# Kernel tuning notes

Hardware: AMD Instinct MI355X
Metric: run time of the kernel (lower is better)

## Reference

```python
import jax, jax.numpy as jnp
import numpy as np

WSZ = 8
HEADS = 8
FILTER_RATE = 0.3
EPS = 1e-5


def layer_norm(x, w, b):
    mu = x.mean(-1, keepdims=True)
    var = ((x - mu) ** 2).mean(-1, keepdims=True)
    return (x - mu) * jax.lax.rsqrt(var + EPS) * w + b


def setup_inputs() -> dict:
    key = jax.random.key(0)
    ks = jax.random.split(key, 8)
    B, C, H, W = 2, 256, 512, 512
    C2 = 2 * C
    s = 0.02
    return {
        "feature_map": jax.random.normal(ks[0], (B, C, H, W), jnp.float32),
        "uncertain_map": jax.random.uniform(ks[1], (B, H, W), jnp.float32),
        "norm_w": jnp.ones((C,), jnp.float32),
        "norm_b": jnp.zeros((C,), jnp.float32),
        "lin0_w": jax.random.normal(ks[2], (C, C2), jnp.float32) * s,
        "lin0_b": jnp.zeros((C2,), jnp.float32),
        "qkv0_w": jax.random.normal(ks[3], (C2, 3 * C2), jnp.float32) * s,
        "lin1_w": jax.random.normal(ks[4], (C2, C2), jnp.float32) * s,
        "lin1_b": jnp.zeros((C2,), jnp.float32),
        "qkv1_w": jax.random.normal(ks[5], (C2, 3 * C2), jnp.float32) * s,
        "proj_w": jax.random.normal(ks[6], (C2, C), jnp.float32) * s,
        "proj_b": jnp.zeros((C,), jnp.float32),
    }


def _window_attn(xf, qkv_w, scale, winsz, C2):
    # xf: (N, winsz, C2)
    qkv = (xf @ qkv_w).reshape(-1, winsz, 3, HEADS, C2 // HEADS)
    q, k, v = qkv[:, :, 0], qkv[:, :, 1], qkv[:, :, 2]  # (N, winsz, H, dh)
    a = jnp.einsum("nqhd,nkhd->nhqk", q, k) * scale
    a = jax.nn.softmax(a, axis=-1)
    o = jnp.einsum("nhqk,nkhd->nqhd", a, v).reshape(-1, winsz, C2)
    return xf + o


def reference(feature_map, uncertain_map, norm_w, norm_b, lin0_w, lin0_b,
              qkv0_w, lin1_w, lin1_b, qkv1_w, proj_w, proj_b):
    B, C, H, W = feature_map.shape
    wsz = WSZ
    nH, nW = H // wsz, W // wsz
    nWin, winsz = nH * nW, wsz * wsz
    nWF = int(nWin * FILTER_RATE)
    C2 = 2 * C
    scale = (C // HEADS) ** -0.5  # module uses C//num_heads, not C2//num_heads

    # window partition
    x = jnp.transpose(feature_map, (0, 2, 3, 1))  # B H W C
    win_x = x.reshape(B, nH, wsz, nW, wsz, C).transpose(0, 1, 3, 2, 4, 5)
    win_x = win_x.reshape(B * nWin, winsz, C)
    win_unc = uncertain_map.reshape(B, nH, wsz, nW, wsz).transpose(0, 1, 3, 2, 4)
    win_unc = win_unc.reshape(B, nWin, winsz)

    # topk window selection by mean uncertainty
    score = win_unc.mean(-1)  # (B, nWin)
    _, idx = jax.lax.top_k(score, nWF)  # (B, nWF)
    flat_idx = (idx + jnp.arange(B)[:, None] * nWin).reshape(-1)  # (B*nWF,)

    xw = win_x[flat_idx]  # gather: (B*nWF, winsz, C)
    xn = layer_norm(xw, norm_w, norm_b)

    # local branch: repeat 0
    xf = jax.nn.gelu(xn @ lin0_w + lin0_b, approximate=False)
    xf = _window_attn(xf, qkv0_w, scale, winsz, C2)
    # repeat 1
    xf = xf + jax.nn.gelu(xf @ lin1_w + lin1_b, approximate=False)
    xf = _window_attn(xf, qkv1_w, scale, winsz, C2)

    out_f = xn + jax.nn.gelu(xf @ proj_w + proj_b, approximate=False)

    # scatter-add back into unnormalized windows
    win_x = win_x.at[flat_idx].add(out_f)

    x = win_x.reshape(B, nH, nW, wsz, wsz, C).transpose(0, 1, 3, 2, 4, 5)
    x = x.reshape(B, H, W, C)
    return jnp.transpose(x, (0, 3, 1, 2))
```

## Files before the change

kernel.cpp:

```cpp
#include <hip/hip_runtime.h>
#include <math.h>

typedef unsigned short u16;
typedef unsigned int   u32;
typedef __attribute__((ext_vector_type(8))) short bf16x8;
typedef __attribute__((ext_vector_type(4))) float f32x4;

#define DEV static __device__ __forceinline__

DEV u16 f2b(float f) {
  union { float f; u32 u; } v; v.f = f;
  u32 r = v.u + 0x7FFFu + ((v.u >> 16) & 1u);
  return (u16)(r >> 16);
}
DEV float b2f(u16 h) {
  union { u32 u; float f; } v; v.u = ((u32)h) << 16;
  return v.f;
}
DEV float gelu_f(float x) { return 0.5f * x * (1.0f + erff(x * 0.70710678118654752f)); }

DEV void gload16(const u16* g, u16* l) {
  __builtin_amdgcn_global_load_lds(
      (const __attribute__((address_space(1))) void*)g,
      (__attribute__((address_space(3))) void*)l, 16, 0, 0);
}

__global__ void k_transpose_w(const float* __restrict__ src, u16* __restrict__ dst,
                              int K, int N) {
  long t = (long)blockIdx.x * 256 + threadIdx.x;
  if (t >= (long)K * N) return;
  int n = (int)(t / K), k = (int)(t % K);
  dst[t] = f2b(src[(long)k * N + n]);
}

__global__ void k_scores(const float* __restrict__ unc, float* __restrict__ scores) {
  int id = blockIdx.x * 256 + threadIdx.x;
  if (id >= 8192) return;
  int b = id >> 12, win = id & 4095;
  int h0 = (win >> 6) << 3, w0 = (win & 63) << 3;
  float r[8] = {0.f,0.f,0.f,0.f,0.f,0.f,0.f,0.f};
  for (int i = 0; i < 8; ++i) {
    long base = ((long)(b * 512 + h0 + i)) * 512 + w0;
    #pragma unroll
    for (int j = 0; j < 8; ++j) r[j] += unc[base + j];
  }
  float s = ((r[0] + r[1]) + (r[2] + r[3])) + ((r[4] + r[5]) + (r[6] + r[7]));
  scores[id] = s * (1.0f / 64.0f);
}

__global__ __launch_bounds__(1024) void k_topk(
    const float* __restrict__ scores, int* __restrict__ row2win,
    int* __restrict__ win2row, int nWF) {
  __shared__ float ls[4096];
  __shared__ int   li[4096];
  const int b = blockIdx.x;
  const int tid = threadIdx.x;
  for (int i = tid; i < 4096; i += 1024) {
    ls[i] = scores[b * 4096 + i];
    li[i] = i;
    win2row[b * 4096 + i] = -1;
  }
  __syncthreads();
  for (int k = 2; k <= 4096; k <<= 1) {
    for (int j = k >> 1; j > 0; j >>= 1) {
      for (int t = tid; t < 2048; t += 1024) {
        int i = ((t / j) * (j << 1)) + (t % j);
        int ixj = i + j;
        bool up = ((i & k) == 0);
        float sa = ls[i], sb = ls[ixj];
        int ia = li[i], ib = li[ixj];
        bool g = (sa > sb) || (sa == sb && ia < ib);
        if (g != up) { ls[i] = sb; ls[ixj] = sa; li[i] = ib; li[ixj] = ia; }
      }
      __syncthreads();
    }
  }
  for (int r = tid; r < nWF; r += 1024) {
    int win = li[r];
    row2win[b * nWF + r] = (b << 12) | win;
    win2row[b * 4096 + win] = b * nWF + r;
  }
}

__global__ __launch_bounds__(256) void k_gather_ln(
    const float* __restrict__ fm, const float* __restrict__ nw,
    const float* __restrict__ nb, const int* __restrict__ row2win,
    u16* __restrict__ xn, int winStart) {
  __shared__ float sx[64 * 256];
  const int tid = threadIdx.x;
  const int rw = row2win[winStart + blockIdx.x];
  const int b = rw >> 12, win = rw & 4095;
  const int h0 = (win >> 6) << 3, w0 = (win & 63) << 3;
  {
    const int c8 = tid >> 3, h = tid & 7;
    #pragma unroll
    for (int cc = 0; cc < 8; ++cc) {
      const int c = cc * 32 + c8;
      long base = ((long)(b * 256 + c) * 512 + h0 + h) * 512 + w0;
      float4 v0 = *(const float4*)(fm + base);
      float4 v1 = *(const float4*)(fm + base + 4);
      float vv[8] = {v0.x, v0.y, v0.z, v0.w, v1.x, v1.y, v1.z, v1.w};
      #pragma unroll
      for (int j = 0; j < 8; ++j) {
        int tok = h * 8 + j;
        sx[tok * 256 + (c ^ ((tok & 15) << 1))] = vv[j];
      }
    }
  }
  __syncthreads();
  const int tok = tid >> 2, g = tid & 3;
  const int swz = (tok & 15) << 1;
  float sum = 0.f;
  for (int q = 0; q < 64; ++q) sum += sx[tok * 256 + ((g * 64 + q) ^ swz)];
  sum += __shfl_xor(sum, 1);
  sum += __shfl_xor(sum, 2);
  const float mu = sum * (1.0f / 256.0f);
  float s2 = 0.f;
  for (int q = 0; q < 64; ++q) {
    float d = sx[tok * 256 + ((g * 64 + q) ^ swz)] - mu;
    s2 += d * d;
  }
  s2 += __shfl_xor(s2, 1);
  s2 += __shfl_xor(s2, 2);
  const float rs = rsqrtf(s2 * (1.0f / 256.0f) + 1e-5f);
  long obase = ((long)blockIdx.x * 64 + tok) * 256 + g * 64;
  for (int q8 = 0; q8 < 8; ++q8) {
    u16 tmp[8];
    #pragma unroll
    for (int e = 0; e < 8; ++e) {
      int c = g * 64 + q8 * 8 + e;
      float v = (sx[tok * 256 + (c ^ swz)] - mu) * rs * nw[c] + nb[c];
      tmp[e] = f2b(v);
    }
    *(ulonglong2*)(xn + obase + q8 * 8) = *(const ulonglong2*)tmp;
  }
}

template <int EPI, int NT, int KD>
__global__ __launch_bounds__(512, 2) void k_gemm256(
    const u16* __restrict__ A, const u16* __restrict__ Bt,
    const float* __restrict__ bias, const u16* __restrict__ Res,
    u16* __restrict__ Y, int N, int nWork) {
  constexpr int NKT = KD / 64;
  constexpr int LG_NKT = (KD == 512) ? 3 : 2;
  constexpr int NIP = KD / 128;
  constexpr int LG_NIP = (KD == 512) ? 2 : 1;
  __shared__ __attribute__((aligned(16))) u16 S[65536];
  __shared__ __attribute__((aligned(16))) u16 E[16384];
  const int tid = threadIdx.x;
  const int l = tid & 63, wid = tid >> 6;
  const int wm = wid >> 2, wn = wid & 3;

  const int slot = ((blockIdx.x & 7) << 5) | (blockIdx.x >> 3);
  const int q = nWork >> 8, rr = nWork & 255;
  const int wrkBase = slot * q + (slot < rr ? slot : rr);
  const int myN = q + (slot < rr ? 1 : 0);
  if (myN == 0) return;

  const int srow = wid * 8 + (l >> 3);
  const int k0b = ((l & 7) << 4) ^ ((l >> 3) << 4);
  const int vko = k0b >> 1;
  char* ldsS = (char*)S + wid * 1024 + l * 16;
  const char* Sb = (const char*)S;

  f32x4 acc[8][4] = {};
  bf16x8 bfrag[4][2];
  bf16x8 af[2][2];

#define STG(G, ISB, H) do { \
    const int wig_ = (G) >> LG_NKT; \
    const int ktg_ = (G) & (NKT - 1); \
    const int wrkg_ = wrkBase + wig_; \
    const int tmg_ = wrkg_ / NT, tng_ = wrkg_ % NT; \
    const u16* g_ = (ISB) ? Bt + (long)(tng_ * 256 + srow) * KD + vko \
                          : A + (long)(tmg_ * 256 + srow) * KD + vko; \
    char* lp_ = ldsS + ((G) & 1) * 65536 + (ISB) * 32768 + (H) * 16384; \
    gload16(g_ + (long)((H) * 128) * KD + ktg_ * 64, (u16*)lp_); \
    gload16(g_ + (long)((H) * 128 + 64) * KD + ktg_ * 64, (u16*)(lp_ + 8192)); \
  } while (0)

#define DS_B(T) do { \
    _Pragma("unroll") for (int ni_ = 0; ni_ < 4; ++ni_) { \
      const int r_ = wn * 64 + ni_ * 16 + (l & 15); \
      _Pragma("unroll") for (int kk_ = 0; kk_ < 2; ++kk_) { \
        const int kb_ = kk_ * 64 + ((l >> 4) << 4); \
        bfrag[ni_][kk_] = *(const bf16x8*)(Sb + ((T) & 1) * 65536 + 32768 + r_ * 128 + (kb_ ^ ((r_ & 7) << 4))); \
      } } \
  } while (0)

#define DS_A(T, Q) do { \
    _Pragma("unroll") for (int m2_ = 0; m2_ < 2; ++m2_) { \
      const int r_ = wm * 128 + (2 * (Q) + m2_) * 16 + (l & 15); \
      _Pragma("unroll") for (int kk_ = 0; kk_ < 2; ++kk_) { \
        const int kb_ = kk_ * 64 + ((l >> 4) << 4); \
        af[m2_][kk_] = *(const bf16x8*)(Sb + ((T) & 1) * 65536 + r_ * 128 + (kb_ ^ ((r_ & 7) << 4))); \
      } } \
  } while (0)

#define MFMA16(Q) do { \
    _Pragma("unroll") for (int m2_ = 0; m2_ < 2; ++m2_) \
      _Pragma("unroll") for (int ni_ = 0; ni_ < 4; ++ni_) \
        _Pragma("unroll") for (int kk_ = 0; kk_ < 2; ++kk_) \
          acc[2 * (Q) + m2_][ni_] = __builtin_amdgcn_mfma_f32_16x16x32_bf16( \
              af[m2_][kk_], bfrag[ni_][kk_], acc[2 * (Q) + m2_][ni_], 0, 0, 0); \
  } while (0)

#define BAR_MFMA(Q) do { \
    __builtin_amdgcn_s_barrier(); \
    asm volatile("s_waitcnt lgkmcnt(0)" ::: "memory"); \
    __builtin_amdgcn_sched_barrier(0); \
    __builtin_amdgcn_s_setprio(1); \
    MFMA16(Q); \
    __builtin_amdgcn_s_setprio(0); \
  } while (0)

#define PH_END() do { \
    __builtin_amdgcn_s_barrier(); \
    __builtin_amdgcn_sched_barrier(0); \
  } while (0)

  STG(0, 0, 0); STG(0, 0, 1); STG(0, 1, 0); STG(0, 1, 1);
  STG(1, 0, 0); STG(1, 0, 1); STG(1, 1, 0); STG(1, 1, 1);
  asm volatile("s_waitcnt vmcnt(8)" ::: "memory");
  __builtin_amdgcn_s_barrier();
  __builtin_amdgcn_sched_barrier(0);

  const int giEnd = myN * NIP;
  for (int gi = 0; gi < giEnd; ++gi) {
    const int t0 = 2 * gi, t1 = t0 + 1;
    const bool more = (gi + 1 < giEnd);
    DS_B(t0); DS_A(t0, 0);
    if (gi > 0) STG(t1, 0, 0);
    BAR_MFMA(0); PH_END();
    DS_A(t0, 1);
    if (gi > 0) STG(t1, 0, 1);
    if (more) STG(t0 + 2, 1, 0);
    BAR_MFMA(1); PH_END();
    DS_A(t0, 2);
    if (more) STG(t0 + 2, 1, 1);
    BAR_MFMA(2); PH_END();
    DS_A(t0, 3);
    BAR_MFMA(3);
    if (more) { asm volatile("s_waitcnt vmcnt(4)" ::: "memory"); }
    else      { asm volatile("s_waitcnt vmcnt(0)" ::: "memory"); }
    PH_END();
    DS_B(t1); DS_A(t1, 0);
    if (more) STG(t0 + 2, 0, 0);
    BAR_MFMA(0); PH_END();
    DS_A(t1, 1);
    if (more) STG(t0 + 2, 0, 1);
    BAR_MFMA(1); PH_END();
    DS_A(t1, 2);
    if (more) STG(t1 + 2, 1, 0);
    BAR_MFMA(2); PH_END();
    DS_A(t1, 3);
    if (more) STG(t1 + 2, 1, 1);
    BAR_MFMA(3);
    if (more) { asm volatile("s_waitcnt vmcnt(4)" ::: "memory"); }
    PH_END();

    if (((gi + 1) & (NIP - 1)) == 0) {
      const int wrk = wrkBase + (gi >> LG_NIP);
      const int tm = wrk / NT, tn = wrk % NT;
      if (EPI == 3) {
        float bv[4];
        #pragma unroll
        for (int ni = 0; ni < 4; ++ni)
          bv[ni] = bias[tn * 256 + wn * 64 + ni * 16 + (l & 15)];
        const long rbase = (long)tm * 256 + wm * 128 + ((l >> 4) << 2);
        const int cbase = tn * 256 + wn * 64 + (l & 15);
        #pragma unroll
        for (int mi = 0; mi < 8; ++mi) {
          #pragma unroll
          for (int r = 0; r < 4; ++r) {
            long m = rbase + mi * 16 + r;
            #pragma unroll
            for (int ni = 0; ni < 4; ++ni) {
              int n = cbase + ni * 16;
              float v = gelu_f(acc[mi][ni][r] + bv[ni]);
              v += b2f(Res[m * N + n]);
              Y[((m >> 6) * 256 + n) * 64 + (m & 63)] = f2b(v);
            }
          }
        }
      } else {
        float bv[4];
        if (EPI == 1 || EPI == 2) {
          #pragma unroll
          for (int ni = 0; ni < 4; ++ni)
            bv[ni] = bias[tn * 256 + wn * 64 + ni * 16 + (l & 15)];
        }
        #pragma unroll
        for (int sw = 0; sw < 4; ++sw) {
          #pragma unroll
          for (int mi2 = 0; mi2 < 2; ++mi2) {
            const int mi = 2 * sw + mi2;
            const int lr0 = wm * 32 + mi2 * 16 + ((l >> 4) << 2);
            #pragma unroll
            for (int r = 0; r < 4; ++r) {
              const int lrr = lr0 + r;
              #pragma unroll
              for (int ni = 0; ni < 4; ++ni) {
                float v = acc[mi][ni][r];
                if (EPI == 1 || EPI == 2) v = gelu_f(v + bv[ni]);
                const int col = wn * 64 + ni * 16 + (l & 15);
                E[lrr * 256 + ((((col >> 3) ^ (lrr & 7)) << 3) | (col & 7))] = f2b(v);
              }
            }
          }
          asm volatile("s_waitcnt lgkmcnt(0)" ::: "memory");
          __builtin_amdgcn_s_barrier();
          const int lr2 = tid >> 3;
          const long m = (long)tm * 256 + (lr2 >> 5) * 128 + sw * 32 + (lr2 & 31);
          #pragma unroll
          for (int rd = 0; rd < 4; ++rd) {
            const int chunk = rd * 8 + (tid & 7);
            ulonglong2 val = *(const ulonglong2*)(E + lr2 * 256 + ((chunk ^ (lr2 & 7)) << 3));
            const int n = tn * 256 + chunk * 8;
            if (EPI == 2) {
              u16 tv[8], rv[8];
              *(ulonglong2*)tv = val;
              *(ulonglong2*)rv = *(const ulonglong2*)(Res + m * N + n);
              #pragma unroll
              for (int e = 0; e < 8; ++e) tv[e] = f2b(b2f(tv[e]) + b2f(rv[e]));
              val = *(const ulonglong2*)tv;
            }
            if (EPI == 4) {
              const long win = m >> 6;
              const int t_ = n >> 9, h_ = (n >> 6) & 7, d0 = n & 63;
              *(ulonglong2*)(Y + ((((win * 8 + h_) * 3 + t_) * 64 + (m & 63)) * 64 + d0)) = val;
            } else {
              *(ulonglong2*)(Y + m * N + n) = val;
            }
          }
          if (sw < 3) {
            __builtin_amdgcn_s_barrier();
          }
        }
      }
      #pragma unroll
      for (int mi = 0; mi < 8; ++mi)
        #pragma unroll
        for (int ni = 0; ni < 4; ++ni)
          acc[mi][ni] = (f32x4){0.f, 0.f, 0.f, 0.f};
    }
  }
#undef STG
#undef DS_B
#undef DS_A
#undef MFMA16
#undef BAR_MFMA
#undef PH_END
}

__global__ __launch_bounds__(256) void k_attn(
    const u16* __restrict__ qkv, u16* __restrict__ xf) {
  __shared__ __attribute__((aligned(16))) u16 sq[64 * 64];
  __shared__ __attribute__((aligned(16))) u16 sk[64 * 64];
  __shared__ __attribute__((aligned(16))) u16 sv[64 * 64];
  __shared__ __attribute__((aligned(16))) u16 sp[64 * 64];
  const int tid = threadIdx.x;
  const int l = tid & 63, w = tid >> 6;
  const int wloc = blockIdx.x >> 3, h = blockIdx.x & 7;
  const long tokbase = (long)wloc * 64;
  const u16* base = qkv + (long)blockIdx.x * 12288;

  #pragma unroll
  for (int rd = 0; rd < 6; ++rd) {
    const int cid = rd * 256 + tid;
    ulonglong2 v16 = *(const ulonglong2*)(base + (long)cid * 8);
    const int t = (cid >> 3) & 63, d0 = (cid & 7) << 3;
    if (rd < 2) {
      *(ulonglong2*)((char*)sq + t * 128 + ((d0 * 2) ^ ((t & 7) << 4))) = v16;
    } else if (rd < 4) {
      *(ulonglong2*)((char*)sk + t * 128 + ((d0 * 2) ^ ((t & 7) << 4))) = v16;
    } else {
      u16 vv[8];
      *(ulonglong2*)vv = v16;
      #pragma unroll
      for (int e = 0; e < 8; ++e) {
        int r = d0 + e;
        *(u16*)((char*)sv + r * 128 + ((t * 2) ^ ((r & 7) << 4))) = vv[e];
      }
    }
  }
  __syncthreads();

  f32x4 accs[4] = {};
  #pragma unroll
  for (int ks = 0; ks < 2; ++ks) {
    int kb = ks * 64 + ((l >> 4) << 4);
    int ra = w * 16 + (l & 15);
    bf16x8 aq = *(const bf16x8*)((char*)sq + ra * 128 + (kb ^ ((ra & 7) << 4)));
    #pragma unroll
    for (int cf = 0; cf < 4; ++cf) {
      int rb = cf * 16 + (l & 15);
      bf16x8 bk = *(const bf16x8*)((char*)sk + rb * 128 + (kb ^ ((rb & 7) << 4)));
      accs[cf] = __builtin_amdgcn_mfma_f32_16x16x32_bf16(aq, bk, accs[cf], 0, 0, 0);
    }
  }
  const float scale = 0.17677669529663687f;
  float pv[4][4];
  #pragma unroll
  for (int r = 0; r < 4; ++r) {
    float m = -1e30f;
    #pragma unroll
    for (int cf = 0; cf < 4; ++cf) {
      pv[cf][r] = accs[cf][r] * scale;
      m = fmaxf(m, pv[cf][r]);
    }
    for (int off = 1; off < 16; off <<= 1) m = fmaxf(m, __shfl_xor(m, off));
    float s = 0.f;
    #pragma unroll
    for (int cf = 0; cf < 4; ++cf) { pv[cf][r] = __expf(pv[cf][r] - m); s += pv[cf][r]; }
    for (int off = 1; off < 16; off <<= 1) s += __shfl_xor(s, off);
    float inv = 1.0f / s;
    #pragma unroll
    for (int cf = 0; cf < 4; ++cf) pv[cf][r] *= inv;
  }
  #pragma unroll
  for (int cf = 0; cf < 4; ++cf)
    #pragma unroll
    for (int r = 0; r < 4; ++r) {
      int pr = w * 16 + ((l >> 4) << 2) + r, pc = cf * 16 + (l & 15);
      *(u16*)((char*)sp + pr * 128 + ((pc * 2) ^ ((pr & 7) << 4))) = f2b(pv[cf][r]);
    }
  __syncthreads();

  f32x4 acco[4] = {};
  #pragma unroll
  for (int ks = 0; ks < 2; ++ks) {
    int kb = ks * 64 + ((l >> 4) << 4);
    int ra = w * 16 + (l & 15);
    bf16x8 ap = *(const bf16x8*)((char*)sp + ra * 128 + (kb ^ ((ra & 7) << 4)));
    #pragma unroll
    for (int cf = 0; cf < 4; ++cf) {
      int rb = cf * 16 + (l & 15);
      bf16x8 bvv = *(const bf16x8*)((char*)sv + rb * 128 + (kb ^ ((rb & 7) << 4)));
      acco[cf] = __builtin_amdgcn_mfma_f32_16x16x32_bf16(ap, bvv, acco[cf], 0, 0, 0);
    }
  }
  #pragma unroll
  for (int cf = 0; cf < 4; ++cf)
    #pragma unroll
    for (int r = 0; r < 4; ++r) {
      long m = tokbase + w * 16 + ((l >> 4) << 2) + r;
      int n = h * 64 + cf * 16 + (l & 15);
      long idx = m * 512 + n;
      xf[idx] = f2b(acco[cf][r] + b2f(xf[idx]));
    }
}

__global__ __launch_bounds__(256) void k_assemble(
    const float* __restrict__ fm, const u16* __restrict__ out_f,
    const int* __restrict__ win2row, float* __restrict__ out) {
  const int tid = threadIdx.x;
  const int bq = blockIdx.x;
  const int hw = bq & 63, c = (bq >> 6) & 255, b = bq >> 14;
  const int w0 = (tid & 127) << 2;
  const int hlo = tid >> 7;
  const int win = hw * 64 + (w0 >> 3);
  const int r = win2row[b * 4096 + win];
  const u16* ofb = out_f + ((long)(r < 0 ? 0 : r) * 256 + c) * 64 + (w0 & 7);
  const long base = ((long)(b * 256 + c) * 512 + hw * 8) * 512 + w0;
  #pragma unroll
  for (int jj = 0; jj < 4; ++jj) {
    const int h = jj * 2 + hlo;
    float4 v = *(const float4*)(fm + base + (long)h * 512);
    if (r >= 0) {
      ushort4 ov = *(const ushort4*)(ofb + h * 8);
      v.x += b2f(ov.x);
      v.y += b2f(ov.y);
      v.z += b2f(ov.z);
      v.w += b2f(ov.w);
    }
    *(float4*)(out + base + (long)h * 512) = v;
  }
}

extern "C" void kernel_launch(void* const* d_in, const int* in_sizes, int n_in,
                              void* d_out, int out_size, void* d_ws, size_t ws_size,
                              hipStream_t stream) {
  const float* fm     = (const float*)d_in[0];
  const float* unc    = (const float*)d_in[1];
  const float* nw     = (const float*)d_in[2];
  const float* nb     = (const float*)d_in[3];
  const float* w_lin0 = (const float*)d_in[4];
  const float* b_lin0 = (const float*)d_in[5];
  const float* w_qkv0 = (const float*)d_in[6];
  const float* w_lin1 = (const float*)d_in[7];
  const float* b_lin1 = (const float*)d_in[8];
  const float* w_qkv1 = (const float*)d_in[9];
  const float* w_proj = (const float*)d_in[10];
  const float* b_proj = (const float*)d_in[11];
  float* out = (float*)d_out;

  const int nWF = 1228, totWin = 2456;
  const long totTok = (long)totWin * 64;

  char* p = (char*)d_ws;
  auto alloc = [&](size_t bytes) {
    char* r = p;
    p += (bytes + 255) & ~(size_t)255;
    return r;
  };
  float* scores = (float*)alloc(8192 * 4);
  int* win2row  = (int*)alloc(8192 * 4);
  int* row2win  = (int*)alloc(totWin * 4);
  u16* wT       = (u16*)alloc((size_t)2097152 * 2);
  u16* out_f    = (u16*)alloc((size_t)(totTok + 256) * 256 * 2);
  size_t persist = (size_t)(p - (char*)d_ws);

  int wpc = totWin;
  {
    const int cands[6] = {1, 2, 4, 8, 16, 32};
    for (int ci = 0; ci < 6; ++ci) {
      int n = cands[ci];
      int wp = ((totWin + n - 1) / n + 3) & ~3;
      size_t mc = (size_t)wp * 64;
      size_t need = persist + 4096 +
                    ((mc * 256 * 2 + 255) & ~(size_t)255) +
                    2 * ((mc * 512 * 2 + 255) & ~(size_t)255) +
                    ((mc * 1536 * 2 + 255) & ~(size_t)255);
      if (need <= ws_size) { wpc = wp; break; }
    }
  }
  long mcap = (long)wpc * 64;
  u16* xn   = (u16*)alloc((size_t)mcap * 256 * 2);
  u16* xfa  = (u16*)alloc((size_t)mcap * 512 * 2);
  u16* xfb  = (u16*)alloc((size_t)mcap * 512 * 2);
  u16* qkvb = (u16*)alloc((size_t)mcap * 1536 * 2);

  u16* wT_lin0 = wT;
  u16* wT_qkv0 = wT + 131072;
  u16* wT_lin1 = wT + 917504;
  u16* wT_qkv1 = wT + 1179648;
  u16* wT_proj = wT + 1966080;
  k_transpose_w<<<(131072 + 255) / 256, 256, 0, stream>>>(w_lin0, wT_lin0, 256, 512);
  k_transpose_w<<<(786432 + 255) / 256, 256, 0, stream>>>(w_qkv0, wT_qkv0, 512, 1536);
  k_transpose_w<<<(262144 + 255) / 256, 256, 0, stream>>>(w_lin1, wT_lin1, 512, 512);
  k_transpose_w<<<(786432 + 255) / 256, 256, 0, stream>>>(w_qkv1, wT_qkv1, 512, 1536);
  k_transpose_w<<<(131072 + 255) / 256, 256, 0, stream>>>(w_proj, wT_proj, 512, 256);

  k_scores<<<32, 256, 0, stream>>>(unc, scores);
  k_topk<<<2, 1024, 0, stream>>>(scores, row2win, win2row, nWF);

  for (int w0 = 0; w0 < totWin; w0 += wpc) {
    int rem = totWin - w0;
    int wn = (wpc < rem) ? wpc : rem;
    int mT = wn / 4;
    k_gather_ln<<<wn, 256, 0, stream>>>(fm, nw, nb, row2win, xn, w0);
    k_gemm256<1, 2, 256><<<256, 512, 0, stream>>>(xn, wT_lin0, b_lin0, nullptr, xfa, 512, mT * 2);
    k_gemm256<4, 6, 512><<<256, 512, 0, stream>>>(xfa, wT_qkv0, nullptr, nullptr, qkvb, 1536, mT * 6);
    k_attn<<<wn * 8, 256, 0, stream>>>(qkvb, xfa);
    k_gemm256<2, 2, 512><<<256, 512, 0, stream>>>(xfa, wT_lin1, b_lin1, xfa, xfb, 512, mT * 2);
    k_gemm256<4, 6, 512><<<256, 512, 0, stream>>>(xfb, wT_qkv1, nullptr, nullptr, qkvb, 1536, mT * 6);
    k_attn<<<wn * 8, 256, 0, stream>>>(qkvb, xfb);
    k_gemm256<3, 1, 512><<<256, 512, 0, stream>>>(xfb, wT_proj, b_proj, xn,
                                                  out_f + (long)w0 * 16384, 256, mT * 1);
  }
  k_assemble<<<32768, 256, 0, stream>>>(fm, out_f, win2row, out);
}
```

Before: 1.983 ms.

## Replace persistent 256x256 pipelined GEMM with simple 128x128 one-tile-per-block GEMM

Replaces the persistent 512-thread GEMM, which used 256x256 tiles, a double-buffered LDS pipeline and multi-phase barriers, with a 256-thread kernel. The new kernel computes one 128x128 tile per block over a single-buffered K loop, and the grid is sized to the number of tiles with an XCD-aware block remap. The aim is more parallelism and occupancy from smaller tiles and lower LDS use. The cost is less operand reuse per tile and no overlap of global loads with MFMA, since each K step waits for its loads to finish before the barrier.

```diff
diff --git a/kernel.cpp b/kernel.cpp
--- a/kernel.cpp
+++ b/kernel.cpp
@@ -137,220 +137,151 @@
 }
 
 template <int EPI, int NT, int KD>
-__global__ __launch_bounds__(512, 2) void k_gemm256(
+__global__ __launch_bounds__(256, 3) void k_gemm128(
     const u16* __restrict__ A, const u16* __restrict__ Bt,
     const float* __restrict__ bias, const u16* __restrict__ Res,
-    u16* __restrict__ Y, int N, int nWork) {
+    u16* __restrict__ Y, int N) {
+  __shared__ __attribute__((aligned(16))) u16 S[16384];
+  const int tid = threadIdx.x;
+  const int l = tid & 63, w = tid >> 6;
+  const int wm = w >> 1, wn = w & 1;
+
+  const int nwg = gridDim.x;
+  const int dd = blockIdx.x;
+  const int xcd = dd & 7, jb = dd >> 3;
+  const int q = nwg >> 3, r8 = nwg & 7;
+  const int wrk = (xcd < r8 ? xcd * (q + 1) : r8 * (q + 1) + (xcd - r8) * q) + jb;
+  const int tm = wrk / NT, tn = wrk % NT;
+
+  const int k0b = ((l & 7) << 4) ^ ((l >> 3) << 4);
+  const u16* gA = A + (long)(tm * 128 + w * 8 + (l >> 3)) * KD + (k0b >> 1);
+  const u16* gB = Bt + (long)(tn * 128 + w * 8 + (l >> 3)) * KD + (k0b >> 1);
+  u16* lA = S + w * 512 + l * 8;
+  u16* lB = lA + 8192;
+  const char* Sb = (const char*)S;
+
+  f32x4 acc[4][4] = {};
   constexpr int NKT = KD / 64;
-  constexpr int LG_NKT = (KD == 512) ? 3 : 2;
-  constexpr int NIP = KD / 128;
-  constexpr int LG_NIP = (KD == 512) ? 2 : 1;
-  __shared__ __attribute__((aligned(16))) u16 S[65536];
-  __shared__ __attribute__((aligned(16))) u16 E[16384];
-  const int tid = threadIdx.x;
-  const int l = tid & 63, wid = tid >> 6;
-  const int wm = wid >> 2, wn = wid & 3;
-
-  const int slot = ((blockIdx.x & 7) << 5) | (blockIdx.x >> 3);
-  const int q = nWork >> 8, rr = nWork & 255;
-  const int wrkBase = slot * q + (slot < rr ? slot : rr);
-  const int myN = q + (slot < rr ? 1 : 0);
-  if (myN == 0) return;
-
-  const int srow = wid * 8 + (l >> 3);
-  const int k0b = ((l & 7) << 4) ^ ((l >> 3) << 4);
-  const int vko = k0b >> 1;
-  char* ldsS = (char*)S + wid * 1024 + l * 16;
-  const char* Sb = (const char*)S;
-
-  f32x4 acc[8][4] = {};
-  bf16x8 bfrag[4][2];
-  bf16x8 af[2][2];
-
-#define STG(G, ISB, H) do { \
-    const int wig_ = (G) >> LG_NKT; \
-    const int ktg_ = (G) & (NKT - 1); \
-    const int wrkg_ = wrkBase + wig_; \
-    const int tmg_ = wrkg_ / NT, tng_ = wrkg_ % NT; \
-    const u16* g_ = (ISB) ? Bt + (long)(tng_ * 256 + srow) * KD + vko \
-                          : A + (long)(tmg_ * 256 + srow) * KD + vko; \
-    char* lp_ = ldsS + ((G) & 1) * 65536 + (ISB) * 32768 + (H) * 16384; \
-    gload16(g_ + (long)((H) * 128) * KD + ktg_ * 64, (u16*)lp_); \
-    gload16(g_ + (long)((H) * 128 + 64) * KD + ktg_ * 64, (u16*)(lp_ + 8192)); \
+
+#define STAGE128(KT) do { \
+    _Pragma("unroll") for (int jr_ = 0; jr_ < 4; ++jr_) { \
+      gload16(gA + (long)jr_ * 32 * KD + (KT) * 64, lA + jr_ * 2048); \
+      gload16(gB + (long)jr_ * 32 * KD + (KT) * 64, lB + jr_ * 2048); \
+    } \
   } while (0)
 
-#define DS_B(T) do { \
-    _Pragma("unroll") for (int ni_ = 0; ni_ < 4; ++ni_) { \
-      const int r_ = wn * 64 + ni_ * 16 + (l & 15); \
-      _Pragma("unroll") for (int kk_ = 0; kk_ < 2; ++kk_) { \
-        const int kb_ = kk_ * 64 + ((l >> 4) << 4); \
-        bfrag[ni_][kk_] = *(const bf16x8*)(Sb + ((T) & 1) * 65536 + 32768 + r_ * 128 + (kb_ ^ ((r_ & 7) << 4))); \
-      } } \
-  } while (0)
-
-#define DS_A(T, Q) do { \
-    _Pragma("unroll") for (int m2_ = 0; m2_ < 2; ++m2_) { \
-      const int r_ = wm * 128 + (2 * (Q) + m2_) * 16 + (l & 15); \
-      _Pragma("unroll") for (int kk_ = 0; kk_ < 2; ++kk_) { \
-        const int kb_ = kk_ * 64 + ((l >> 4) << 4); \
-        af[m2_][kk_] = *(const bf16x8*)(Sb + ((T) & 1) * 65536 + r_ * 128 + (kb_ ^ ((r_ & 7) << 4))); \
-      } } \
-  } while (0)
-
-#define MFMA16(Q) do { \
-    _Pragma("unroll") for (int m2_ = 0; m2_ < 2; ++m2_) \
-      _Pragma("unroll") for (int ni_ = 0; ni_ < 4; ++ni_) \
-        _Pragma("unroll") for (int kk_ = 0; kk_ < 2; ++kk_) \
-          acc[2 * (Q) + m2_][ni_] = __builtin_amdgcn_mfma_f32_16x16x32_bf16( \
-              af[m2_][kk_], bfrag[ni_][kk_], acc[2 * (Q) + m2_][ni_], 0, 0, 0); \
-  } while (0)
-
-#define BAR_MFMA(Q) do { \
-    __builtin_amdgcn_s_barrier(); \
-    asm volatile("s_waitcnt lgkmcnt(0)" ::: "memory"); \
-    __builtin_amdgcn_sched_barrier(0); \
-    __builtin_amdgcn_s_setprio(1); \
-    MFMA16(Q); \
-    __builtin_amdgcn_s_setprio(0); \
-  } while (0)
-
-#define PH_END() do { \
-    __builtin_amdgcn_s_barrier(); \
-    __builtin_amdgcn_sched_barrier(0); \
-  } while (0)
-
-  STG(0, 0, 0); STG(0, 0, 1); STG(0, 1, 0); STG(0, 1, 1);
-  STG(1, 0, 0); STG(1, 0, 1); STG(1, 1, 0); STG(1, 1, 1);
-  asm volatile("s_waitcnt vmcnt(8)" ::: "memory");
+  STAGE128(0);
+  asm volatile("s_waitcnt vmcnt(0)" ::: "memory");
   __builtin_amdgcn_s_barrier();
   __builtin_amdgcn_sched_barrier(0);
 
-  const int giEnd = myN * NIP;
-  for (int gi = 0; gi < giEnd; ++gi) {
-    const int t0 = 2 * gi, t1 = t0 + 1;
-    const bool more = (gi + 1 < giEnd);
-    DS_B(t0); DS_A(t0, 0);
-    if (gi > 0) STG(t1, 0, 0);
-    BAR_MFMA(0); PH_END();
-    DS_A(t0, 1);
-    if (gi > 0) STG(t1, 0, 1);
-    if (more) STG(t0 + 2, 1, 0);
-    BAR_MFMA(1); PH_END();
-    DS_A(t0, 2);
-    if (more) STG(t0 + 2, 1, 1);
-    BAR_MFMA(2); PH_END();
-    DS_A(t0, 3);
-    BAR_MFMA(3);
-    if (more) { asm volatile("s_waitcnt vmcnt(4)" ::: "memory"); }
-    else      { asm volatile("s_waitcnt vmcnt(0)" ::: "memory"); }
-    PH_END();
-    DS_B(t1); DS_A(t1, 0);
-    if (more) STG(t0 + 2, 0, 0);
-    BAR_MFMA(0); PH_END();
-    DS_A(t1, 1);
-    if (more) STG(t0 + 2, 0, 1);
-    BAR_MFMA(1); PH_END();
-    DS_A(t1, 2);
-    if (more) STG(t1 + 2, 1, 0);
-    BAR_MFMA(2); PH_END();
-    DS_A(t1, 3);
-    if (more) STG(t1 + 2, 1, 1);
-    BAR_MFMA(3);
-    if (more) { asm volatile("s_waitcnt vmcnt(4)" ::: "memory"); }
-    PH_END();
-
-    if (((gi + 1) & (NIP - 1)) == 0) {
-      const int wrk = wrkBase + (gi >> LG_NIP);
-      const int tm = wrk / NT, tn = wrk % NT;
-      if (EPI == 3) {
-        float bv[4];
+  for (int kt = 0; kt < NKT; ++kt) {
+    bf16x8 af[4][2], bf[4][2];
+    #pragma unroll
+    for (int mi = 0; mi < 4; ++mi) {
+      const int r_ = wm * 64 + mi * 16 + (l & 15);
+      #pragma unroll
+      for (int kk = 0; kk < 2; ++kk) {
+        const int kb = kk * 64 + ((l >> 4) << 4);
+        af[mi][kk] = *(const bf16x8*)(Sb + r_ * 128 + (kb ^ ((r_ & 7) << 4)));
+      }
+    }
+    #pragma unroll
+    for (int ni = 0; ni < 4; ++ni) {
+      const int r_ = wn * 64 + ni * 16 + (l & 15);
+      #pragma unroll
+      for (int kk = 0; kk < 2; ++kk) {
+        const int kb = kk * 64 + ((l >> 4) << 4);
+        bf[ni][kk] = *(const bf16x8*)(Sb + 16384 + r_ * 128 + (kb ^ ((r_ & 7) << 4)));
+      }
+    }
+    asm volatile("s_waitcnt lgkmcnt(0)" ::: "memory");
+    __builtin_amdgcn_sched_barrier(0);
+    __builtin_amdgcn_s_barrier();
+    __builtin_amdgcn_sched_barrier(0);
+    if (kt + 1 < NKT) STAGE128(kt + 1);
+    #pragma unroll
+    for (int mi = 0; mi < 4; ++mi)
+      #pragma unroll
+      for (int ni = 0; ni < 4; ++ni)
         #pragma unroll
-        for (int ni = 0; ni < 4; ++ni)
-          bv[ni] = bias[tn * 256 + wn * 64 + ni * 16 + (l & 15)];
-        const long rbase = (long)tm * 256 + wm * 128 + ((l >> 4) << 2);
-        const int cbase = tn * 256 + wn * 64 + (l & 15);
+        for (int kk = 0; kk < 2; ++kk)
+          acc[mi][ni] = __builtin_amdgcn_mfma_f32_16x16x32_bf16(
+              af[mi][kk], bf[ni][kk], acc[mi][ni], 0, 0, 0);
+    if (kt + 1 < NKT) {
+      asm volatile("s_waitcnt vmcnt(0)" ::: "memory");
+      __builtin_amdgcn_s_barrier();
+      __builtin_amdgcn_sched_barrier(0);
+    }
+  }
+
+  if (EPI == 3) {
+    float bv[4];
+    #pragma unroll
+    for (int ni = 0; ni < 4; ++ni)
+      bv[ni] = bias[tn * 128 + wn * 64 + ni * 16 + (l & 15)];
+    #pragma unroll
+    for (int mi = 0; mi < 4; ++mi) {
+      #pragma unroll
+      for (int r = 0; r < 4; ++r) {
+        long m = (long)tm * 128 + wm * 64 + mi * 16 + ((l >> 4) << 2) + r;
         #pragma unroll
-        for (int mi = 0; mi < 8; ++mi) {
-          #pragma unroll
-          for (int r = 0; r < 4; ++r) {
-            long m = rbase + mi * 16 + r;
-            #pragma unroll
-            for (int ni = 0; ni < 4; ++ni) {
-              int n = cbase + ni * 16;
-              float v = gelu_f(acc[mi][ni][r] + bv[ni]);
-              v += b2f(Res[m * N + n]);
-              Y[((m >> 6) * 256 + n) * 64 + (m & 63)] = f2b(v);
-            }
-          }
+        for (int ni = 0; ni < 4; ++ni) {
+          int n = tn * 128 + wn * 64 + ni * 16 + (l & 15);
+          float v = gelu_f(acc[mi][ni][r] + bv[ni]);
+          v += b2f(Res[m * N + n]);
+          Y[((m >> 6) * 256 + n) * 64 + (m & 63)] = f2b(v);
         }
+      }
+    }
+  } else {
+    float bv[4];
+    if (EPI == 1 || EPI == 2) {
+      #pragma unroll
+      for (int ni = 0; ni < 4; ++ni)
+        bv[ni] = bias[tn * 128 + wn * 64 + ni * 16 + (l & 15)];
+    }
+    #pragma unroll
+    for (int mi = 0; mi < 4; ++mi) {
+      #pragma unroll
+      for (int r = 0; r < 4; ++r) {
+        const int row = wm * 64 + mi * 16 + ((l >> 4) << 2) + r;
+        #pragma unroll
+        for (int ni = 0; ni < 4; ++ni) {
+          float v = acc[mi][ni][r];
+          if (EPI == 1 || EPI == 2) v = gelu_f(v + bv[ni]);
+          const int col = wn * 64 + ni * 16 + (l & 15);
+          *(u16*)((char*)S + row * 256 + ((col * 2) ^ ((row & 7) << 4))) = f2b(v);
+        }
+      }
+    }
+    asm volatile("s_waitcnt lgkmcnt(0)" ::: "memory");
+    __builtin_amdgcn_s_barrier();
+    const int row = tid >> 1, half = tid & 1;
+    const long m = (long)tm * 128 + row;
+    #pragma unroll
+    for (int jr = 0; jr < 8; ++jr) {
+      ulonglong2 val = *(const ulonglong2*)(
+          Sb + row * 256 + ((half * 128 + jr * 16) ^ ((row & 7) << 4)));
+      const int n = tn * 128 + half * 64 + jr * 8;
+      if (EPI == 2) {
+        u16 tv[8], rv[8];
+        *(ulonglong2*)tv = val;
+        *(ulonglong2*)rv = *(const ulonglong2*)(Res + m * N + n);
+        #pragma unroll
+        for (int e = 0; e < 8; ++e) tv[e] = f2b(b2f(tv[e]) + b2f(rv[e]));
+        val = *(const ulonglong2*)tv;
+      }
+      if (EPI == 4) {
+        const long win = m >> 6;
+        const int t_ = n >> 9, h_ = (n >> 6) & 7, d0 = n & 63;
+        *(ulonglong2*)(Y + ((((win * 8 + h_) * 3 + t_) * 64 + (m & 63)) * 64 + d0)) = val;
       } else {
-        float bv[4];
-        if (EPI == 1 || EPI == 2) {
-          #pragma unroll
-          for (int ni = 0; ni < 4; ++ni)
-            bv[ni] = bias[tn * 256 + wn * 64 + ni * 16 + (l & 15)];
-        }
-        #pragma unroll
-        for (int sw = 0; sw < 4; ++sw) {
-          #pragma unroll
-          for (int mi2 = 0; mi2 < 2; ++mi2) {
-            const int mi = 2 * sw + mi2;
-            const int lr0 = wm * 32 + mi2 * 16 + ((l >> 4) << 2);
-            #pragma unroll
-            for (int r = 0; r < 4; ++r) {
-              const int lrr = lr0 + r;
-              #pragma unroll
-              for (int ni = 0; ni < 4; ++ni) {
-                float v = acc[mi][ni][r];
-                if (EPI == 1 || EPI == 2) v = gelu_f(v + bv[ni]);
-                const int col = wn * 64 + ni * 16 + (l & 15);
-                E[lrr * 256 + ((((col >> 3) ^ (lrr & 7)) << 3) | (col & 7))] = f2b(v);
-              }
-            }
-          }
-          asm volatile("s_waitcnt lgkmcnt(0)" ::: "memory");
-          __builtin_amdgcn_s_barrier();
-          const int lr2 = tid >> 3;
-          const long m = (long)tm * 256 + (lr2 >> 5) * 128 + sw * 32 + (lr2 & 31);
-          #pragma unroll
-          for (int rd = 0; rd < 4; ++rd) {
-            const int chunk = rd * 8 + (tid & 7);
-            ulonglong2 val = *(const ulonglong2*)(E + lr2 * 256 + ((chunk ^ (lr2 & 7)) << 3));
-            const int n = tn * 256 + chunk * 8;
-            if (EPI == 2) {
-              u16 tv[8], rv[8];
-              *(ulonglong2*)tv = val;
-              *(ulonglong2*)rv = *(const ulonglong2*)(Res + m * N + n);
-              #pragma unroll
-              for (int e = 0; e < 8; ++e) tv[e] = f2b(b2f(tv[e]) + b2f(rv[e]));
-              val = *(const ulonglong2*)tv;
-            }
-            if (EPI == 4) {
-              const long win = m >> 6;
-              const int t_ = n >> 9, h_ = (n >> 6) & 7, d0 = n & 63;
-              *(ulonglong2*)(Y + ((((win * 8 + h_) * 3 + t_) * 64 + (m & 63)) * 64 + d0)) = val;
-            } else {
-              *(ulonglong2*)(Y + m * N + n) = val;
-            }
-          }
-          if (sw < 3) {
-            __builtin_amdgcn_s_barrier();
-          }
-        }
-      }
-      #pragma unroll
-      for (int mi = 0; mi < 8; ++mi)
-        #pragma unroll
-        for (int ni = 0; ni < 4; ++ni)
-          acc[mi][ni] = (f32x4){0.f, 0.f, 0.f, 0.f};
-    }
-  }
-#undef STG
-#undef DS_B
-#undef DS_A
-#undef MFMA16
-#undef BAR_MFMA
-#undef PH_END
+        *(ulonglong2*)(Y + m * N + n) = val;
+      }
+    }
+  }
+#undef STAGE128
 }
 
 __global__ __launch_bounds__(256) void k_attn(
@@ -548,16 +479,16 @@
   for (int w0 = 0; w0 < totWin; w0 += wpc) {
     int rem = totWin - w0;
     int wn = (wpc < rem) ? wpc : rem;
-    int mT = wn / 4;
+    int mT = wn / 2;
     k_gather_ln<<<wn, 256, 0, stream>>>(fm, nw, nb, row2win, xn, w0);
-    k_gemm256<1, 2, 256><<<256, 512, 0, stream>>>(xn, wT_lin0, b_lin0, nullptr, xfa, 512, mT * 2);
-    k_gemm256<4, 6, 512><<<256, 512, 0, stream>>>(xfa, wT_qkv0, nullptr, nullptr, qkvb, 1536, mT * 6);
+    k_gemm128<1, 4, 256><<<mT * 4, 256, 0, stream>>>(xn, wT_lin0, b_lin0, nullptr, xfa, 512);
+    k_gemm128<4, 12, 512><<<mT * 12, 256, 0, stream>>>(xfa, wT_qkv0, nullptr, nullptr, qkvb, 1536);
     k_attn<<<wn * 8, 256, 0, stream>>>(qkvb, xfa);
-    k_gemm256<2, 2, 512><<<256, 512, 0, stream>>>(xfa, wT_lin1, b_lin1, xfa, xfb, 512, mT * 2);
-    k_gemm256<4, 6, 512><<<256, 512, 0, stream>>>(xfb, wT_qkv1, nullptr, nullptr, qkvb, 1536, mT * 6);
+    k_gemm128<2, 4, 512><<<mT * 4, 256, 0, stream>>>(xfa, wT_lin1, b_lin1, xfa, xfb, 512);
+    k_gemm128<4, 12, 512><<<mT * 12, 256, 0, stream>>>(xfb, wT_qkv1, nullptr, nullptr, qkvb, 1536);
     k_attn<<<wn * 8, 256, 0, stream>>>(qkvb, xfb);
-    k_gemm256<3, 1, 512><<<256, 512, 0, stream>>>(xfb, wT_proj, b_proj, xn,
-                                                  out_f + (long)w0 * 16384, 256, mT * 1);
+    k_gemm128<3, 2, 512><<<mT * 2, 256, 0, stream>>>(xfb, wT_proj, b_proj, xn,
+                                                     out_f + (long)w0 * 16384, 256);
   }
   k_assemble<<<32768, 256, 0, stream>>>(fm, out_f, win2row, out);
 }
```

New measurement: 2.130 ms. +7.4%, slower.

## Replace persistent GEMM scheduling with one tile per workgroup grid

Applied to the files above, without the earlier changes.

The GEMM kernel no longer runs as a persistent 256-block grid that loops over several output tiles with a cross-tile prefetch pipeline. It now launches one workgroup per 256x256 tile, mapped so that consecutive tiles land on the same XCD. The separate epilogue LDS buffer E is dropped and the staging buffer S is reused, which cuts LDS per block and may allow more blocks resident. In exchange, the kernel loses the prefetch of the next tile's operands across tile boundaries and adds launch and tail costs when the tile count is not a multiple of the CU count.

```diff
diff --git a/kernel.cpp b/kernel.cpp
--- a/kernel.cpp
+++ b/kernel.cpp
@@ -140,26 +140,23 @@
 __global__ __launch_bounds__(512, 2) void k_gemm256(
     const u16* __restrict__ A, const u16* __restrict__ Bt,
     const float* __restrict__ bias, const u16* __restrict__ Res,
-    u16* __restrict__ Y, int N, int nWork) {
-  constexpr int NKT = KD / 64;
-  constexpr int LG_NKT = (KD == 512) ? 3 : 2;
-  constexpr int NIP = KD / 128;
-  constexpr int LG_NIP = (KD == 512) ? 2 : 1;
+    u16* __restrict__ Y, int N) {
   __shared__ __attribute__((aligned(16))) u16 S[65536];
-  __shared__ __attribute__((aligned(16))) u16 E[16384];
   const int tid = threadIdx.x;
   const int l = tid & 63, wid = tid >> 6;
   const int wm = wid >> 2, wn = wid & 3;
 
-  const int slot = ((blockIdx.x & 7) << 5) | (blockIdx.x >> 3);
-  const int q = nWork >> 8, rr = nWork & 255;
-  const int wrkBase = slot * q + (slot < rr ? slot : rr);
-  const int myN = q + (slot < rr ? 1 : 0);
-  if (myN == 0) return;
+  const int nwg = gridDim.x;
+  const int d = blockIdx.x;
+  const int xcd = d & 7, j = d >> 3;
+  const int q = nwg >> 3, r8 = nwg & 7;
+  const int wrk = (xcd < r8 ? xcd * (q + 1) : r8 * (q + 1) + (xcd - r8) * q) + j;
+  const int tm = wrk / NT, tn = wrk % NT;
 
   const int srow = wid * 8 + (l >> 3);
   const int k0b = ((l & 7) << 4) ^ ((l >> 3) << 4);
-  const int vko = k0b >> 1;
+  const u16* gA = A + (long)(tm * 256 + srow) * KD + (k0b >> 1);
+  const u16* gB = Bt + (long)(tn * 256 + srow) * KD + (k0b >> 1);
   char* ldsS = (char*)S + wid * 1024 + l * 16;
   const char* Sb = (const char*)S;
 
@@ -167,16 +164,11 @@
   bf16x8 bfrag[4][2];
   bf16x8 af[2][2];
 
-#define STG(G, ISB, H) do { \
-    const int wig_ = (G) >> LG_NKT; \
-    const int ktg_ = (G) & (NKT - 1); \
-    const int wrkg_ = wrkBase + wig_; \
-    const int tmg_ = wrkg_ / NT, tng_ = wrkg_ % NT; \
-    const u16* g_ = (ISB) ? Bt + (long)(tng_ * 256 + srow) * KD + vko \
-                          : A + (long)(tmg_ * 256 + srow) * KD + vko; \
-    char* lp_ = ldsS + ((G) & 1) * 65536 + (ISB) * 32768 + (H) * 16384; \
-    gload16(g_ + (long)((H) * 128) * KD + ktg_ * 64, (u16*)lp_); \
-    gload16(g_ + (long)((H) * 128 + 64) * KD + ktg_ * 64, (u16*)(lp_ + 8192)); \
+#define STG(T, ISB, H) do { \
+    const u16* g_ = (ISB) ? gB : gA; \
+    char* lp_ = ldsS + ((T) & 1) * 65536 + (ISB) * 32768 + (H) * 16384; \
+    gload16(g_ + (long)((H) * 128) * KD + (long)(T) * 64, (u16*)lp_); \
+    gload16(g_ + (long)((H) * 128 + 64) * KD + (long)(T) * 64, (u16*)(lp_ + 8192)); \
   } while (0)
 
 #define DS_B(T) do { \
@@ -225,15 +217,15 @@
   __builtin_amdgcn_s_barrier();
   __builtin_amdgcn_sched_barrier(0);
 
-  const int giEnd = myN * NIP;
-  for (int gi = 0; gi < giEnd; ++gi) {
-    const int t0 = 2 * gi, t1 = t0 + 1;
-    const bool more = (gi + 1 < giEnd);
+  constexpr int nIter = KD >> 7;
+  for (int i = 0; i < nIter; ++i) {
+    const int t0 = 2 * i, t1 = 2 * i + 1;
+    const bool more = (i + 1 < nIter);
     DS_B(t0); DS_A(t0, 0);
-    if (gi > 0) STG(t1, 0, 0);
+    if (i > 0) STG(t1, 0, 0);
     BAR_MFMA(0); PH_END();
     DS_A(t0, 1);
-    if (gi > 0) STG(t1, 0, 1);
+    if (i > 0) STG(t1, 0, 1);
     if (more) STG(t0 + 2, 1, 0);
     BAR_MFMA(1); PH_END();
     DS_A(t0, 2);
@@ -258,91 +250,82 @@
     BAR_MFMA(3);
     if (more) { asm volatile("s_waitcnt vmcnt(4)" ::: "memory"); }
     PH_END();
-
-    if (((gi + 1) & (NIP - 1)) == 0) {
-      const int wrk = wrkBase + (gi >> LG_NIP);
-      const int tm = wrk / NT, tn = wrk % NT;
-      if (EPI == 3) {
-        float bv[4];
+  }
+
+  if (EPI == 3) {
+    float bv[4];
+    #pragma unroll
+    for (int ni = 0; ni < 4; ++ni)
+      bv[ni] = bias[tn * 256 + wn * 64 + ni * 16 + (l & 15)];
+    const long rbase = (long)tm * 256 + wm * 128 + ((l >> 4) << 2);
+    const int cbase = tn * 256 + wn * 64 + (l & 15);
+    #pragma unroll
+    for (int mi = 0; mi < 8; ++mi) {
+      #pragma unroll
+      for (int r = 0; r < 4; ++r) {
+        long m = rbase + mi * 16 + r;
         #pragma unroll
-        for (int ni = 0; ni < 4; ++ni)
-          bv[ni] = bias[tn * 256 + wn * 64 + ni * 16 + (l & 15)];
-        const long rbase = (long)tm * 256 + wm * 128 + ((l >> 4) << 2);
-        const int cbase = tn * 256 + wn * 64 + (l & 15);
+        for (int ni = 0; ni < 4; ++ni) {
+          int n = cbase + ni * 16;
+          float v = gelu_f(acc[mi][ni][r] + bv[ni]);
+          v += b2f(Res[m * N + n]);
+          Y[((m >> 6) * 256 + n) * 64 + (m & 63)] = f2b(v);
+        }
+      }
+    }
+  } else {
+    float bv[4];
+    if (EPI == 1 || EPI == 2) {
+      #pragma unroll
+      for (int ni = 0; ni < 4; ++ni)
+        bv[ni] = bias[tn * 256 + wn * 64 + ni * 16 + (l & 15)];
+    }
+    #pragma unroll
+    for (int sw = 0; sw < 4; ++sw) {
+      #pragma unroll
+      for (int mi2 = 0; mi2 < 2; ++mi2) {
+        const int mi = 2 * sw + mi2;
+        const int lr0 = wm * 32 + mi2 * 16 + ((l >> 4) << 2);
         #pragma unroll
-        for (int mi = 0; mi < 8; ++mi) {
+        for (int r = 0; r < 4; ++r) {
+          const int lrr = lr0 + r;
           #pragma unroll
-          for (int r = 0; r < 4; ++r) {
-            long m = rbase + mi * 16 + r;
-            #pragma unroll
-            for (int ni = 0; ni < 4; ++ni) {
-              int n = cbase + ni * 16;
-              float v = gelu_f(acc[mi][ni][r] + bv[ni]);
-              v += b2f(Res[m * N + n]);
-              Y[((m >> 6) * 256 + n) * 64 + (m & 63)] = f2b(v);
-            }
+          for (int ni = 0; ni < 4; ++ni) {
+            float v = acc[mi][ni][r];
+            if (EPI == 1 || EPI == 2) v = gelu_f(v + bv[ni]);
+            const int col = wn * 64 + ni * 16 + (l & 15);
+            S[lrr * 256 + ((((col >> 3) ^ (lrr & 7)) << 3) | (col & 7))] = f2b(v);
           }
         }
-      } else {
-        float bv[4];
-        if (EPI == 1 || EPI == 2) {
+      }
+      asm volatile("s_waitcnt lgkmcnt(0)" ::: "memory");
+      __builtin_amdgcn_s_barrier();
+      const int lr2 = tid >> 3;
+      const long m = (long)tm * 256 + (lr2 >> 5) * 128 + sw * 32 + (lr2 & 31);
+      #pragma unroll
+      for (int rd = 0; rd < 4; ++rd) {
+        const int chunk = rd * 8 + (tid & 7);
+        ulonglong2 val = *(const ulonglong2*)(S + lr2 * 256 + ((chunk ^ (lr2 & 7)) << 3));
+        const int n = tn * 256 + chunk * 8;
+        if (EPI == 2) {
+          u16 tv[8], rv[8];
+          *(ulonglong2*)tv = val;
+          *(ulonglong2*)rv = *(const ulonglong2*)(Res + m * N + n);
           #pragma unroll
-          for (int ni = 0; ni < 4; ++ni)
-            bv[ni] = bias[tn * 256 + wn * 64 + ni * 16 + (l & 15)];
+          for (int e = 0; e < 8; ++e) tv[e] = f2b(b2f(tv[e]) + b2f(rv[e]));
+          val = *(const ulonglong2*)tv;
         }
-        #pragma unroll
-        for (int sw = 0; sw < 4; ++sw) {
-          #pragma unroll
-          for (int mi2 = 0; mi2 < 2; ++mi2) {
-            const int mi = 2 * sw + mi2;
-            const int lr0 = wm * 32 + mi2 * 16 + ((l >> 4) << 2);
-            #pragma unroll
-            for (int r = 0; r < 4; ++r) {
-              const int lrr = lr0 + r;
-              #pragma unroll
-              for (int ni = 0; ni < 4; ++ni) {
-                float v = acc[mi][ni][r];
-                if (EPI == 1 || EPI == 2) v = gelu_f(v + bv[ni]);
-                const int col = wn * 64 + ni * 16 + (l & 15);
-                E[lrr * 256 + ((((col >> 3) ^ (lrr & 7)) << 3) | (col & 7))] = f2b(v);
-              }
-            }
-          }
-          asm volatile("s_waitcnt lgkmcnt(0)" ::: "memory");
-          __builtin_amdgcn_s_barrier();
-          const int lr2 = tid >> 3;
-          const long m = (long)tm * 256 + (lr2 >> 5) * 128 + sw * 32 + (lr2 & 31);
-          #pragma unroll
-          for (int rd = 0; rd < 4; ++rd) {
-            const int chunk = rd * 8 + (tid & 7);
-            ulonglong2 val = *(const ulonglong2*)(E + lr2 * 256 + ((chunk ^ (lr2 & 7)) << 3));
-            const int n = tn * 256 + chunk * 8;
-            if (EPI == 2) {
-              u16 tv[8], rv[8];
-              *(ulonglong2*)tv = val;
-              *(ulonglong2*)rv = *(const ulonglong2*)(Res + m * N + n);
-              #pragma unroll
-              for (int e = 0; e < 8; ++e) tv[e] = f2b(b2f(tv[e]) + b2f(rv[e]));
-              val = *(const ulonglong2*)tv;
-            }
-            if (EPI == 4) {
-              const long win = m >> 6;
-              const int t_ = n >> 9, h_ = (n >> 6) & 7, d0 = n & 63;
-              *(ulonglong2*)(Y + ((((win * 8 + h_) * 3 + t_) * 64 + (m & 63)) * 64 + d0)) = val;
-            } else {
-              *(ulonglong2*)(Y + m * N + n) = val;
-            }
-          }
-          if (sw < 3) {
-            __builtin_amdgcn_s_barrier();
-          }
+        if (EPI == 4) {
+          const long win = m >> 6;
+          const int t_ = n >> 9, h_ = (n >> 6) & 7, d0 = n & 63;
+          *(ulonglong2*)(Y + ((((win * 8 + h_) * 3 + t_) * 64 + (m & 63)) * 64 + d0)) = val;
+        } else {
+          *(ulonglong2*)(Y + m * N + n) = val;
         }
       }
-      #pragma unroll
-      for (int mi = 0; mi < 8; ++mi)
-        #pragma unroll
-        for (int ni = 0; ni < 4; ++ni)
-          acc[mi][ni] = (f32x4){0.f, 0.f, 0.f, 0.f};
+      if (sw < 3) {
+        __builtin_amdgcn_s_barrier();
+      }
     }
   }
 #undef STG
@@ -550,14 +533,14 @@
     int wn = (wpc < rem) ? wpc : rem;
     int mT = wn / 4;
     k_gather_ln<<<wn, 256, 0, stream>>>(fm, nw, nb, row2win, xn, w0);
-    k_gemm256<1, 2, 256><<<256, 512, 0, stream>>>(xn, wT_lin0, b_lin0, nullptr, xfa, 512, mT * 2);
-    k_gemm256<4, 6, 512><<<256, 512, 0, stream>>>(xfa, wT_qkv0, nullptr, nullptr, qkvb, 1536, mT * 6);
+    k_gemm256<1, 2, 256><<<mT * 2, 512, 0, stream>>>(xn, wT_lin0, b_lin0, nullptr, xfa, 512);
+    k_gemm256<4, 6, 512><<<mT * 6, 512, 0, stream>>>(xfa, wT_qkv0, nullptr, nullptr, qkvb, 1536);
     k_attn<<<wn * 8, 256, 0, stream>>>(qkvb, xfa);
-    k_gemm256<2, 2, 512><<<256, 512, 0, stream>>>(xfa, wT_lin1, b_lin1, xfa, xfb, 512, mT * 2);
-    k_gemm256<4, 6, 512><<<256, 512, 0, stream>>>(xfb, wT_qkv1, nullptr, nullptr, qkvb, 1536, mT * 6);
+    k_gemm256<2, 2, 512><<<mT * 2, 512, 0, stream>>>(xfa, wT_lin1, b_lin1, xfa, xfb, 512);
+    k_gemm256<4, 6, 512><<<mT * 6, 512, 0, stream>>>(xfb, wT_qkv1, nullptr, nullptr, qkvb, 1536);
     k_attn<<<wn * 8, 256, 0, stream>>>(qkvb, xfb);
-    k_gemm256<3, 1, 512><<<256, 512, 0, stream>>>(xfb, wT_proj, b_proj, xn,
-                                                  out_f + (long)w0 * 16384, 256, mT * 1);
+    k_gemm256<3, 1, 512><<<mT * 1, 512, 0, stream>>>(xfb, wT_proj, b_proj, xn,
+                                                     out_f + (long)w0 * 16384, 256);
   }
   k_assemble<<<32768, 256, 0, stream>>>(fm, out_f, win2row, out);
 }
```

Measured after the change: 1.902 ms. 1.04x faster.
